# Kernel optimization log

Hardware: AMD Instinct MI355X
Metric: run time of the kernel (lower is better)

## Reference

```python
import jax, jax.numpy as jnp
import numpy as np

N = 100000   # nodes
E = 1600000  # edges
IN = 512     # in_channels
H = 256      # hidden_channels
C = 40       # out_channels
BITS = 8     # INT8 fake quantization


def fake_quant(x, bits=BITS):
    """Symmetric per-tensor quantize-dequantize with straight-through estimator."""
    qmax = float(2 ** (bits - 1) - 1)
    scale = jnp.max(jnp.abs(x)) / qmax + 1e-12
    q = jnp.clip(jnp.round(x / scale), -qmax - 1.0, qmax) * scale
    # STE: forward = q, backward = identity
    return x + jax.lax.stop_gradient(q - x)


def quant_linear(x, w, b):
    # LinearQuantized: fake-quant inputs and weights, fp accumulate
    return fake_quant(x) @ fake_quant(w).T + b


def gcn_propagate(x, edge_index):
    """Symmetric-normalized sparse propagation: out = D^-1/2 A D^-1/2 x."""
    src, dst = edge_index[0], edge_index[1]
    deg = jax.ops.segment_sum(jnp.ones((E,), x.dtype), dst, num_segments=N)
    dinv = jnp.where(deg > 0, jax.lax.rsqrt(jnp.maximum(deg, 1.0)), 0.0)
    coef = dinv[src] * dinv[dst]                     # [E]
    msgs = x[src] * coef[:, None]                    # [E, C]
    return jax.ops.segment_sum(msgs, dst, num_segments=N)  # [N, C]


def setup_inputs() -> dict:
    key = jax.random.key(0)
    ks = jax.random.split(key, 6)
    x = jax.random.normal(ks[0], (N, IN), jnp.float32)
    edge_index = jax.random.randint(ks[1], (2, E), 0, N, dtype=jnp.int32)
    w1 = jax.random.normal(ks[2], (H, IN), jnp.float32) * (1.0 / np.sqrt(IN))
    b1 = jnp.zeros((H,), jnp.float32)
    w2 = jax.random.normal(ks[3], (C, H), jnp.float32) * (1.0 / np.sqrt(H))
    b2 = jnp.zeros((C,), jnp.float32)
    return {"x": x, "edge_index": edge_index, "w1": w1, "b1": b1, "w2": w2, "b2": b2}


def reference(x, edge_index, w1, b1, w2, b2):
    # dropout: identity in eval mode
    h = jax.nn.relu(quant_linear(x, w1, b1))         # [N, H]
    z = quant_linear(h, w2, b2)                      # [N, C]
    z = gcn_propagate(z, edge_index)                 # [N, C]
    return jax.nn.log_softmax(z, axis=1)
```

## Files before the change

### kernel.cpp

```cpp
#include <hip/hip_runtime.h>
#include <hip/hip_bf16.h>
#include <hip/hip_fp16.h>
#include <stdint.h>
#include <stddef.h>

#define NN   100000
#define NE   1600000
#define INC  512
#define HID  256
#define OC   40
#define OCP  48

#define LDS1 144
#define LDSB2 272

#define NBKT ((NN + 255) / 256)
#define NMT1 ((NN + 127) / 128)
#define GEMM1_BLKS (((NMT1 + 7) / 8) * 16)

#define ABS_X_BLKS  2048
#define ABS_W1_BLKS 128
#define ABS_W2_BLKS 16
#define ABS_TOT     (ABS_X_BLKS + ABS_W1_BLKS + ABS_W2_BLKS)
#define CHIST_BLKS  256
#define QW1_BLKS    128
#define QW2_BLKS    16
#define QW_TOT      (QW1_BLKS + QW2_BLKS)
#define BIN_BLOCKS  400
#define BIN_EPB     (NE / BIN_BLOCKS)

typedef float  f32x4  __attribute__((ext_vector_type(4)));
typedef int    i32x4  __attribute__((ext_vector_type(4)));
typedef _Float16 f16x8 __attribute__((ext_vector_type(8)));

__device__ unsigned g_amax_bits[4];
__device__ float    g_dinv[NN];
__device__ signed char g_qw1[HID * INC];
__device__ signed char g_qw2[OCP * HID];
__device__ _Float16 g_h[(size_t)NN * HID];
__device__ float    g_z[(size_t)NN * OC];
__device__ unsigned g_chist[NBKT];
__device__ unsigned g_cstart[NBKT + 1];
__device__ unsigned g_ccur[NBKT];
__device__ uint2    g_bin[NE];
__device__ unsigned g_rowstart[NN + 1];
__device__ int      g_csr_src[NE];

__device__ __forceinline__ float quantf(float v, float rs) {
    return fminf(fmaxf(rintf(v * rs), -128.0f), 127.0f);
}
__device__ __forceinline__ int pack4(float a, float b, float c, float d, float rs) {
    int q0 = (int)quantf(a, rs), q1 = (int)quantf(b, rs);
    int q2 = (int)quantf(c, rs), q3 = (int)quantf(d, rs);
    return (q0 & 255) | ((q1 & 255) << 8) | ((q2 & 255) << 16) | ((q3 & 255) << 24);
}
__device__ __forceinline__ i32x4 pack16(f32x4 v0, f32x4 v1, f32x4 v2, f32x4 v3, float rs) {
    i32x4 o;
    o[0] = pack4(v0.x, v0.y, v0.z, v0.w, rs);
    o[1] = pack4(v1.x, v1.y, v1.z, v1.w, rs);
    o[2] = pack4(v2.x, v2.y, v2.z, v2.w, rs);
    o[3] = pack4(v3.x, v3.y, v3.z, v3.w, rs);
    return o;
}

__global__ void init_kernel() {
    int idx = blockIdx.x * blockDim.x + threadIdx.x;
    int stride = gridDim.x * blockDim.x;
    for (int i = idx; i < NBKT; i += stride) g_chist[i] = 0u;
    for (int i = idx; i < (OCP * HID) / 4; i += stride) ((int*)g_qw2)[i] = 0;
    if (idx < 4) g_amax_bits[idx] = 0u;
}

__global__ void __launch_bounds__(256) absmax_chist_kernel(const float* __restrict__ x,
                                                           const float* __restrict__ w1,
                                                           const float* __restrict__ w2,
                                                           const int* __restrict__ ei) {
    __shared__ unsigned shist[NBKT];
    __shared__ float sm[4];
    int b = blockIdx.x;
    int t = threadIdx.x;
    if (b < ABS_TOT) {
        const float* src; int n4, slot, bbase, nb;
        if (b < ABS_X_BLKS) {
            src = x;  n4 = (NN * INC) / 4;  slot = 0; bbase = 0;                       nb = ABS_X_BLKS;
        } else if (b < ABS_X_BLKS + ABS_W1_BLKS) {
            src = w1; n4 = (HID * INC) / 4; slot = 1; bbase = ABS_X_BLKS;              nb = ABS_W1_BLKS;
        } else {
            src = w2; n4 = (OC * HID) / 4;  slot = 2; bbase = ABS_X_BLKS + ABS_W1_BLKS; nb = ABS_W2_BLKS;
        }
        int idx = (b - bbase) * 256 + t;
        int stride = nb * 256;
        const f32x4* s4 = (const f32x4*)src;
        float m = 0.0f;
        for (int i = idx; i < n4; i += stride) {
            f32x4 v = s4[i];
            m = fmaxf(m, fmaxf(fmaxf(fabsf(v.x), fabsf(v.y)),
                               fmaxf(fabsf(v.z), fabsf(v.w))));
        }
#pragma unroll
        for (int off = 32; off > 0; off >>= 1) m = fmaxf(m, __shfl_xor(m, off, 64));
        if ((t & 63) == 0) sm[t >> 6] = m;
        __syncthreads();
        if (t == 0) {
            float mm = fmaxf(fmaxf(sm[0], sm[1]), fmaxf(sm[2], sm[3]));
            atomicMax(&g_amax_bits[slot], __float_as_uint(mm));
        }
    } else {
        const int* dst = ei + NE;
        for (int i = t; i < NBKT; i += 256) shist[i] = 0u;
        __syncthreads();
        int idx = (b - ABS_TOT) * 256 + t;
        int stride = CHIST_BLKS * 256;
        for (int e = idx; e < NE; e += stride) atomicAdd(&shist[dst[e] >> 8], 1u);
        __syncthreads();
        for (int i = t; i < NBKT; i += 256) {
            unsigned c = shist[i];
            if (c) atomicAdd(&g_chist[i], c);
        }
    }
}

__global__ void cscan_kernel() {
    int t = threadIdx.x;
    unsigned v = (t < NBKT) ? g_chist[t] : 0u;
    int lane = t & 63, wv = t >> 6;
    unsigned sc = v;
#pragma unroll
    for (int off = 1; off < 64; off <<= 1) {
        unsigned n = __shfl_up(sc, off, 64);
        if (lane >= off) sc += n;
    }
    __shared__ unsigned ws[8];
    if (lane == 63) ws[wv] = sc;
    __syncthreads();
    unsigned woff = 0;
    for (int w = 0; w < 8; w++) if (w < wv) woff += ws[w];
    unsigned excl = woff + sc - v;
    if (t < NBKT) { g_cstart[t] = excl; g_ccur[t] = excl; }
    if (t == 0) g_cstart[NBKT] = NE;
}

__global__ void __launch_bounds__(256) quant_bin_kernel(const float* __restrict__ w1,
                                                        const float* __restrict__ w2,
                                                        const int* __restrict__ ei) {
    __shared__ unsigned hist[NBKT];
    __shared__ unsigned base[NBKT];
    int b = blockIdx.x;
    int t = threadIdx.x;
    if (b < QW_TOT) {
        const float* src; int* dst; int nint, slot, bbase, nb;
        if (b < QW1_BLKS) { src = w1; dst = (int*)g_qw1; nint = (HID * INC) / 4; slot = 1; bbase = 0;        nb = QW1_BLKS; }
        else              { src = w2; dst = (int*)g_qw2; nint = (OC * HID) / 4;  slot = 2; bbase = QW1_BLKS; nb = QW2_BLKS; }
        float rs = 1.0f / (__uint_as_float(g_amax_bits[slot]) / 127.0f + 1e-12f);
        int idx = (b - bbase) * 256 + t;
        int stride = nb * 256;
        for (int i = idx; i < nint; i += stride) {
            f32x4 v = *(const f32x4*)(src + (size_t)i * 4);
            dst[i] = pack4(v.x, v.y, v.z, v.w, rs);
        }
    } else {
        const int* srcp = ei;
        const int* dstp = ei + NE;
        int bb = b - QW_TOT;
        int e0 = bb * BIN_EPB, e1 = e0 + BIN_EPB;
        for (int i = t; i < NBKT; i += 256) hist[i] = 0u;
        __syncthreads();
        for (int e = e0 + t; e < e1; e += 256) atomicAdd(&hist[dstp[e] >> 8], 1u);
        __syncthreads();
        for (int i = t; i < NBKT; i += 256) {
            unsigned c = hist[i];
            base[i] = c ? atomicAdd(&g_ccur[i], c) : 0u;
            hist[i] = 0u;
        }
        __syncthreads();
        for (int e = e0 + t; e < e1; e += 256) {
            int d = dstp[e], s = srcp[e];
            int bk = d >> 8;
            unsigned r = atomicAdd(&hist[bk], 1u);
            g_bin[base[bk] + r] = make_uint2((unsigned)s, (unsigned)d);
        }
    }
}

__global__ void __launch_bounds__(256) gemm1_local_kernel(const float* __restrict__ x,
                                                          const float* __restrict__ b1) {
    __shared__ char lA[2][128 * LDS1];
    __shared__ char lB[2][128 * LDS1];
    int t = threadIdx.x;
    if (blockIdx.x >= GEMM1_BLKS) {
        int b = blockIdx.x - GEMM1_BLKS;
        unsigned* hist = (unsigned*)lA;
        unsigned* curs = hist + 256;
        unsigned* wsum = curs + 256;
        unsigned e0 = g_cstart[b], e1 = g_cstart[b + 1];
        hist[t] = 0u;
        __syncthreads();
        for (unsigned e = e0 + t; e < e1; e += 256) atomicAdd(&hist[g_bin[e].y & 255], 1u);
        __syncthreads();
        unsigned v = hist[t];
        int lane = t & 63, wv = t >> 6;
        unsigned sc = v;
#pragma unroll
        for (int off = 1; off < 64; off <<= 1) {
            unsigned n = __shfl_up(sc, off, 64);
            if (lane >= off) sc += n;
        }
        if (lane == 63) wsum[wv] = sc;
        __syncthreads();
        unsigned woff = 0;
        for (int w = 0; w < 4; w++) if (w < wv) woff += wsum[w];
        unsigned excl = woff + sc - v;
        int node = b * 256 + t;
        if (node < NN) {
            g_rowstart[node] = e0 + excl;
            g_dinv[node] = v ? rsqrtf((float)v) : 0.0f;
        }
        if (b == 0 && t == 0) g_rowstart[NN] = NE;
        curs[t] = excl;
        __syncthreads();
        for (unsigned e = e0 + t; e < e1; e += 256) {
            uint2 ed = g_bin[e];
            unsigned r = atomicAdd(&curs[ed.y & 255], 1u);
            g_csr_src[e0 + r] = (int)ed.x;
        }
        return;
    }
    int group = blockIdx.x >> 4;
    int ntile = (blockIdx.x >> 3) & 1;
    int mtile = group * 8 + (blockIdx.x & 7);
    if (mtile >= NMT1) return;
    int lane = t & 63, wv = t >> 6;
    int quad = lane >> 4, l16 = lane & 15;
    int mq = wv >> 1, nq = wv & 1;

    int srow = t >> 3;
    int sch  = t & 7;

    float rsx = 1.0f / (__uint_as_float(g_amax_bits[0]) / 127.0f + 1e-12f);

    const float* xb[4];
    const signed char* wb[4];
#pragma unroll
    for (int p = 0; p < 4; p++) {
        int gr = mtile * 128 + p * 32 + srow; if (gr >= NN) gr = NN - 1;
        xb[p] = x + (size_t)gr * INC + sch * 16;
        wb[p] = g_qw1 + (size_t)(ntile * 128 + p * 32 + srow) * INC + sch * 16;
    }

    f32x4 ra[4][4];
    i32x4 bv[4];
#pragma unroll
    for (int p = 0; p < 4; p++) {
#pragma unroll
        for (int k = 0; k < 4; k++) ra[p][k] = ((const f32x4*)xb[p])[k];
        bv[p] = *(const i32x4*)(wb[p]);
    }

    i32x4 acc[4][4] = {};
#pragma unroll 1
    for (int kit = 0; kit < 4; kit++) {
        int bs = kit & 1;
#pragma unroll
        for (int p = 0; p < 4; p++) {
            int row = p * 32 + srow;
            i32x4 oa = pack16(ra[p][0], ra[p][1], ra[p][2], ra[p][3], rsx);
            *(i32x4*)(lA[bs] + row * LDS1 + sch * 16) = oa;
            *(i32x4*)(lB[bs] + row * LDS1 + sch * 16) = bv[p];
        }
        if (kit + 1 < 4) {
#pragma unroll
            for (int p = 0; p < 4; p++) {
#pragma unroll
                for (int k = 0; k < 4; k++) ra[p][k] = ((const f32x4*)(xb[p] + (kit + 1) * 128))[k];
                bv[p] = *(const i32x4*)(wb[p] + (kit + 1) * 128);
            }
        }
        __syncthreads();
#pragma unroll
        for (int ks = 0; ks < 2; ks++) {
            int cs = ks * 64 + quad * 16;
            i32x4 a[4], b[4];
#pragma unroll
            for (int i = 0; i < 4; i++)
                a[i] = *(const i32x4*)(lA[bs] + (mq * 64 + i * 16 + l16) * LDS1 + cs);
#pragma unroll
            for (int j = 0; j < 4; j++)
                b[j] = *(const i32x4*)(lB[bs] + (nq * 64 + j * 16 + l16) * LDS1 + cs);
#pragma unroll
            for (int i = 0; i < 4; i++)
#pragma unroll
                for (int j = 0; j < 4; j++)
                    acc[i][j] = __builtin_amdgcn_mfma_i32_16x16x64_i8(a[i], b[j], acc[i][j], 0, 0, 0);
        }
    }
    float s = (__uint_as_float(g_amax_bits[0]) / 127.0f + 1e-12f)
            * (__uint_as_float(g_amax_bits[1]) / 127.0f + 1e-12f);
    float lmax = 0.0f;
#pragma unroll
    for (int j = 0; j < 4; j++) {
        int col = ntile * 128 + nq * 64 + j * 16 + l16;
        float bias = b1[col];
#pragma unroll
        for (int i = 0; i < 4; i++) {
#pragma unroll
            for (int r = 0; r < 4; r++) {
                int grow = mtile * 128 + mq * 64 + i * 16 + quad * 4 + r;
                float v = fmaxf(s * (float)acc[i][j][r] + bias, 0.0f);
                lmax = fmaxf(lmax, v);
                if (grow < NN) g_h[(size_t)grow * HID + col] = (_Float16)v;
            }
        }
    }
#pragma unroll
    for (int off = 32; off > 0; off >>= 1) lmax = fmaxf(lmax, __shfl_xor(lmax, off, 64));
    if (lane == 0) atomicMax(&g_amax_bits[3], __float_as_uint(lmax));
}

__launch_bounds__(256)
__global__ void gemm2_kernel(const float* __restrict__ b2) {
    __shared__ char lB2[OCP * LDSB2];
    __shared__ char lA2[128 * LDS1];
    int t = threadIdx.x;
    int mtile = blockIdx.x;
    int lane = t & 63, wv = t >> 6;
    int quad = lane >> 4, l16 = lane & 15;

#pragma unroll
    for (int p = 0; p < 3; p++) {
        int ci = p * 256 + t;
        int row = ci >> 4, ch = ci & 15;
        *(i32x4*)(lB2 + row * LDSB2 + ch * 16) =
            *(const i32x4*)(g_qw2 + row * 256 + ch * 16);
    }

    float scale_h = __uint_as_float(g_amax_bits[3]) / 127.0f + 1e-12f;
    float rs = 1.0f / scale_h;
    int srow = t >> 3, sch = t & 7;
    const _Float16* hbase[4];
#pragma unroll
    for (int p = 0; p < 4; p++) {
        int gr = mtile * 128 + p * 32 + srow; if (gr >= NN) gr = NN - 1;
        hbase[p] = g_h + (size_t)gr * HID + sch * 16;
    }

    i32x4 acc[2][3] = {};
#pragma unroll 1
    for (int kit = 0; kit < 2; kit++) {
        if (kit) __syncthreads();
#pragma unroll
        for (int p = 0; p < 4; p++) {
            int row = p * 32 + srow;
            const _Float16* hp = hbase[p] + kit * 128;
            f16x8 v0 = *(const f16x8*)(hp);
            f16x8 v1 = *(const f16x8*)(hp + 8);
            i32x4 o;
            o[0] = pack4((float)v0[0], (float)v0[1], (float)v0[2], (float)v0[3], rs);
            o[1] = pack4((float)v0[4], (float)v0[5], (float)v0[6], (float)v0[7], rs);
            o[2] = pack4((float)v1[0], (float)v1[1], (float)v1[2], (float)v1[3], rs);
            o[3] = pack4((float)v1[4], (float)v1[5], (float)v1[6], (float)v1[7], rs);
            *(i32x4*)(lA2 + row * LDS1 + sch * 16) = o;
        }
        __syncthreads();
#pragma unroll
        for (int ks = 0; ks < 2; ks++) {
            int cs = ks * 64 + quad * 16;
            i32x4 a[2], b[3];
#pragma unroll
            for (int i = 0; i < 2; i++)
                a[i] = *(const i32x4*)(lA2 + (wv * 32 + i * 16 + l16) * LDS1 + cs);
#pragma unroll
            for (int j = 0; j < 3; j++)
                b[j] = *(const i32x4*)(lB2 + (j * 16 + l16) * LDSB2 + kit * 128 + cs);
#pragma unroll
            for (int i = 0; i < 2; i++)
#pragma unroll
                for (int j = 0; j < 3; j++)
                    acc[i][j] = __builtin_amdgcn_mfma_i32_16x16x64_i8(a[i], b[j], acc[i][j], 0, 0, 0);
        }
    }
    float s = scale_h * (__uint_as_float(g_amax_bits[2]) / 127.0f + 1e-12f);
#pragma unroll
    for (int j = 0; j < 3; j++) {
        int col = j * 16 + l16;
        float bias = (col < OC) ? b2[col] : 0.0f;
#pragma unroll
        for (int i = 0; i < 2; i++) {
#pragma unroll
            for (int r = 0; r < 4; r++) {
                int grow = mtile * 128 + wv * 32 + i * 16 + quad * 4 + r;
                if (col < OC && grow < NN)
                    g_z[(size_t)grow * OC + col] = s * (float)acc[i][j][r] + bias;
            }
        }
    }
}

__launch_bounds__(256)
__global__ void gather_kernel(float* __restrict__ out) {
    int node = (blockIdx.x * 256 + threadIdx.x) >> 6;
    int lane = threadIdx.x & 63;
    if (node >= NN) return;
    unsigned e0 = g_rowstart[node], e1 = g_rowstart[node + 1];
    float dinvd = g_dinv[node];
    bool ch = (lane < OC);
    float acc0 = 0.0f, acc1 = 0.0f;
    unsigned e = e0;
    for (; e + 8 <= e1; e += 8) {
        int s0 = g_csr_src[e],     s1 = g_csr_src[e + 1];
        int s2 = g_csr_src[e + 2], s3 = g_csr_src[e + 3];
        int s4 = g_csr_src[e + 4], s5 = g_csr_src[e + 5];
        int s6 = g_csr_src[e + 6], s7 = g_csr_src[e + 7];
        float c0 = g_dinv[s0], c1 = g_dinv[s1], c2 = g_dinv[s2], c3 = g_dinv[s3];
        float c4 = g_dinv[s4], c5 = g_dinv[s5], c6 = g_dinv[s6], c7 = g_dinv[s7];
        float z0 = ch ? g_z[(size_t)s0 * OC + lane] : 0.0f;
        float z1 = ch ? g_z[(size_t)s1 * OC + lane] : 0.0f;
        float z2 = ch ? g_z[(size_t)s2 * OC + lane] : 0.0f;
        float z3 = ch ? g_z[(size_t)s3 * OC + lane] : 0.0f;
        float z4 = ch ? g_z[(size_t)s4 * OC + lane] : 0.0f;
        float z5 = ch ? g_z[(size_t)s5 * OC + lane] : 0.0f;
        float z6 = ch ? g_z[(size_t)s6 * OC + lane] : 0.0f;
        float z7 = ch ? g_z[(size_t)s7 * OC + lane] : 0.0f;
        acc0 += (z0 * c0 + z1 * c1) + (z2 * c2 + z3 * c3);
        acc1 += (z4 * c4 + z5 * c5) + (z6 * c6 + z7 * c7);
    }
    for (; e + 4 <= e1; e += 4) {
        int s0 = g_csr_src[e],     s1 = g_csr_src[e + 1];
        int s2 = g_csr_src[e + 2], s3 = g_csr_src[e + 3];
        float c0 = g_dinv[s0], c1 = g_dinv[s1], c2 = g_dinv[s2], c3 = g_dinv[s3];
        float z0 = ch ? g_z[(size_t)s0 * OC + lane] : 0.0f;
        float z1 = ch ? g_z[(size_t)s1 * OC + lane] : 0.0f;
        float z2 = ch ? g_z[(size_t)s2 * OC + lane] : 0.0f;
        float z3 = ch ? g_z[(size_t)s3 * OC + lane] : 0.0f;
        acc0 += (z0 * c0 + z1 * c1) + (z2 * c2 + z3 * c3);
    }
    for (; e < e1; e++) {
        int s0 = g_csr_src[e];
        float z0 = ch ? g_z[(size_t)s0 * OC + lane] : 0.0f;
        acc1 += z0 * g_dinv[s0];
    }
    float acc = (acc0 + acc1) * dinvd;
    float m = ch ? acc : -1e30f;
#pragma unroll
    for (int off = 32; off > 0; off >>= 1) m = fmaxf(m, __shfl_xor(m, off, 64));
    float ex = ch ? __expf(acc - m) : 0.0f;
    float ssum = ex;
#pragma unroll
    for (int off = 32; off > 0; off >>= 1) ssum += __shfl_xor(ssum, off, 64);
    float lg = __logf(ssum);
    if (ch) out[(size_t)node * OC + lane] = acc - m - lg;
}

extern "C" void kernel_launch(void* const* d_in, const int* in_sizes, int n_in,
                              void* d_out, int out_size, void* d_ws, size_t ws_size,
                              hipStream_t stream) {
    const float* x  = (const float*)d_in[0];
    const int*   ei = (const int*)d_in[1];
    const float* w1 = (const float*)d_in[2];
    const float* b1 = (const float*)d_in[3];
    const float* w2 = (const float*)d_in[4];
    const float* b2 = (const float*)d_in[5];
    float* out = (float*)d_out;
    (void)d_ws; (void)ws_size; (void)in_sizes; (void)n_in; (void)out_size;

    init_kernel<<<64, 256, 0, stream>>>();
    absmax_chist_kernel<<<ABS_TOT + CHIST_BLKS, 256, 0, stream>>>(x, w1, w2, ei);
    cscan_kernel<<<1, 512, 0, stream>>>();
    quant_bin_kernel<<<QW_TOT + BIN_BLOCKS, 256, 0, stream>>>(w1, w2, ei);
    gemm1_local_kernel<<<GEMM1_BLKS + NBKT, 256, 0, stream>>>(x, b1);
    gemm2_kernel<<<(NN + 127) / 128, 256, 0, stream>>>(b2);
    gather_kernel<<<(NN + 3) / 4, 256, 0, stream>>>(out);
}
```

Before: 540.1 us.

## Load GEMM1 MFMA operands directly from global memory, bypassing LDS staging

Replaces the shared-memory double-buffered staging in the INT8 GEMM1 path with direct per-wave register loads of x and quantized W1 fragments in MFMA layout, quantizing x in registers. This removes LDS writes/reads and block barriers and shrinks shared memory use to the small CSR-build buffers. In exchange each x row is loaded and quantized by two waves, doubling global reads of the fp32 input, with smaller, less coalesced per-lane accesses.

```diff
diff --git a/kernel.cpp b/kernel.cpp
--- a/kernel.cpp
+++ b/kernel.cpp
@@ -184,20 +184,18 @@
 
 __global__ void __launch_bounds__(256) gemm1_local_kernel(const float* __restrict__ x,
                                                           const float* __restrict__ b1) {
-    __shared__ char lA[2][128 * LDS1];
-    __shared__ char lB[2][128 * LDS1];
+    __shared__ unsigned sh_hist[256];
+    __shared__ unsigned sh_curs[256];
+    __shared__ unsigned sh_wsum[4];
     int t = threadIdx.x;
     if (blockIdx.x >= GEMM1_BLKS) {
         int b = blockIdx.x - GEMM1_BLKS;
-        unsigned* hist = (unsigned*)lA;
-        unsigned* curs = hist + 256;
-        unsigned* wsum = curs + 256;
         unsigned e0 = g_cstart[b], e1 = g_cstart[b + 1];
-        hist[t] = 0u;
-        __syncthreads();
-        for (unsigned e = e0 + t; e < e1; e += 256) atomicAdd(&hist[g_bin[e].y & 255], 1u);
-        __syncthreads();
-        unsigned v = hist[t];
+        sh_hist[t] = 0u;
+        __syncthreads();
+        for (unsigned e = e0 + t; e < e1; e += 256) atomicAdd(&sh_hist[g_bin[e].y & 255], 1u);
+        __syncthreads();
+        unsigned v = sh_hist[t];
         int lane = t & 63, wv = t >> 6;
         unsigned sc = v;
 #pragma unroll
@@ -205,10 +203,10 @@
             unsigned n = __shfl_up(sc, off, 64);
             if (lane >= off) sc += n;
         }
-        if (lane == 63) wsum[wv] = sc;
+        if (lane == 63) sh_wsum[wv] = sc;
         __syncthreads();
         unsigned woff = 0;
-        for (int w = 0; w < 4; w++) if (w < wv) woff += wsum[w];
+        for (int w = 0; w < 4; w++) if (w < wv) woff += sh_wsum[w];
         unsigned excl = woff + sc - v;
         int node = b * 256 + t;
         if (node < NN) {
@@ -216,11 +214,11 @@
             g_dinv[node] = v ? rsqrtf((float)v) : 0.0f;
         }
         if (b == 0 && t == 0) g_rowstart[NN] = NE;
-        curs[t] = excl;
+        sh_curs[t] = excl;
         __syncthreads();
         for (unsigned e = e0 + t; e < e1; e += 256) {
             uint2 ed = g_bin[e];
-            unsigned r = atomicAdd(&curs[ed.y & 255], 1u);
+            unsigned r = atomicAdd(&sh_curs[ed.y & 255], 1u);
             g_csr_src[e0 + r] = (int)ed.x;
         }
         return;
@@ -233,65 +231,48 @@
     int quad = lane >> 4, l16 = lane & 15;
     int mq = wv >> 1, nq = wv & 1;
 
-    int srow = t >> 3;
-    int sch  = t & 7;
-
     float rsx = 1.0f / (__uint_as_float(g_amax_bits[0]) / 127.0f + 1e-12f);
 
-    const float* xb[4];
+    const float* xa[4];
     const signed char* wb[4];
 #pragma unroll
-    for (int p = 0; p < 4; p++) {
-        int gr = mtile * 128 + p * 32 + srow; if (gr >= NN) gr = NN - 1;
-        xb[p] = x + (size_t)gr * INC + sch * 16;
-        wb[p] = g_qw1 + (size_t)(ntile * 128 + p * 32 + srow) * INC + sch * 16;
+    for (int i = 0; i < 4; i++) {
+        int gr = mtile * 128 + mq * 64 + i * 16 + l16; if (gr >= NN) gr = NN - 1;
+        xa[i] = x + (size_t)gr * INC + quad * 16;
+        wb[i] = g_qw1 + (size_t)(ntile * 128 + nq * 64 + i * 16 + l16) * INC + quad * 16;
     }
 
     f32x4 ra[4][4];
-    i32x4 bv[4];
-#pragma unroll
-    for (int p = 0; p < 4; p++) {
-#pragma unroll
-        for (int k = 0; k < 4; k++) ra[p][k] = ((const f32x4*)xb[p])[k];
-        bv[p] = *(const i32x4*)(wb[p]);
+    i32x4 rb[4];
+#pragma unroll
+    for (int i = 0; i < 4; i++) {
+#pragma unroll
+        for (int k = 0; k < 4; k++) ra[i][k] = ((const f32x4*)xa[i])[k];
+        rb[i] = *(const i32x4*)(wb[i]);
     }
 
     i32x4 acc[4][4] = {};
 #pragma unroll 1
-    for (int kit = 0; kit < 4; kit++) {
-        int bs = kit & 1;
-#pragma unroll
-        for (int p = 0; p < 4; p++) {
-            int row = p * 32 + srow;
-            i32x4 oa = pack16(ra[p][0], ra[p][1], ra[p][2], ra[p][3], rsx);
-            *(i32x4*)(lA[bs] + row * LDS1 + sch * 16) = oa;
-            *(i32x4*)(lB[bs] + row * LDS1 + sch * 16) = bv[p];
-        }
-        if (kit + 1 < 4) {
-#pragma unroll
-            for (int p = 0; p < 4; p++) {
-#pragma unroll
-                for (int k = 0; k < 4; k++) ra[p][k] = ((const f32x4*)(xb[p] + (kit + 1) * 128))[k];
-                bv[p] = *(const i32x4*)(wb[p] + (kit + 1) * 128);
+    for (int g = 0; g < 8; g++) {
+        i32x4 a[4], b[4];
+#pragma unroll
+        for (int i = 0; i < 4; i++) {
+            a[i] = pack16(ra[i][0], ra[i][1], ra[i][2], ra[i][3], rsx);
+            b[i] = rb[i];
+        }
+        if (g + 1 < 8) {
+#pragma unroll
+            for (int i = 0; i < 4; i++) {
+#pragma unroll
+                for (int k = 0; k < 4; k++) ra[i][k] = ((const f32x4*)(xa[i] + (g + 1) * 64))[k];
+                rb[i] = *(const i32x4*)(wb[i] + (g + 1) * 64);
             }
         }
-        __syncthreads();
-#pragma unroll
-        for (int ks = 0; ks < 2; ks++) {
-            int cs = ks * 64 + quad * 16;
-            i32x4 a[4], b[4];
-#pragma unroll
-            for (int i = 0; i < 4; i++)
-                a[i] = *(const i32x4*)(lA[bs] + (mq * 64 + i * 16 + l16) * LDS1 + cs);
+#pragma unroll
+        for (int i = 0; i < 4; i++)
 #pragma unroll
             for (int j = 0; j < 4; j++)
-                b[j] = *(const i32x4*)(lB[bs] + (nq * 64 + j * 16 + l16) * LDS1 + cs);
-#pragma unroll
-            for (int i = 0; i < 4; i++)
-#pragma unroll
-                for (int j = 0; j < 4; j++)
-                    acc[i][j] = __builtin_amdgcn_mfma_i32_16x16x64_i8(a[i], b[j], acc[i][j], 0, 0, 0);
-        }
+                acc[i][j] = __builtin_amdgcn_mfma_i32_16x16x64_i8(a[i], b[j], acc[i][j], 0, 0, 0);
     }
     float s = (__uint_as_float(g_amax_bits[0]) / 127.0f + 1e-12f)
             * (__uint_as_float(g_amax_bits[1]) / 127.0f + 1e-12f);
```

Measured after the change: 612.9 us. 13.5% more time.
